# Optimization experiments

Hardware: AMD Instinct MI355X
Metric: run time of the kernel (lower is better)

The kernel has to match this reference:

```python
import jax, jax.numpy as jnp
import numpy as np

BLOCK_SPLIT = (4, 4, 4)
GRID = 256
N_BLOCK = 64
BX = GRID // 4  # 64, per-block grid resolution along each axis
N_PTS = 4_194_304


def setup_inputs() -> dict:
    key = jax.random.key(0)
    k1, k2 = jax.random.split(key)
    aabb = jnp.array([[-1.5, -1.5, -1.5], [1.5, 1.5, 1.5]], dtype=jnp.float32)
    # points roughly inside the aabb
    xyz_sampled = jax.random.uniform(k1, (N_PTS, 3), dtype=jnp.float32) * 3.0 - 1.5
    alpha_volume = jax.random.uniform(k2, (GRID, GRID, GRID), dtype=jnp.float32)
    # per-block domains (as kilonerf global_to_local expects): block AABBs
    idx = np.stack(np.meshgrid(np.arange(4), np.arange(4), np.arange(4), indexing='ij'), -1).reshape(-1, 3)
    voxel = np.array([3.0 / 4.0] * 3)
    dmin = (-1.5 + idx * voxel).astype(np.float32)
    dmax = (dmin + voxel).astype(np.float32)
    return {"xyz_sampled": xyz_sampled, "aabb": aabb, "alpha_volume": alpha_volume,
            "domain_min": jnp.asarray(dmin), "domain_max": jnp.asarray(dmax)}


def _sample_alpha(xyz, aabb, alpha_volume, dmin, dmax):
    bs = jnp.asarray(BLOCK_SPLIT, jnp.float32)
    voxel = (aabb[1] - aabb[0]) / bs                      # per-block world size
    idx3 = jnp.floor((xyz - aabb[0]) / voxel).astype(jnp.int32)
    idx3 = jnp.clip(idx3, 0, jnp.array(BLOCK_SPLIT, jnp.int32) - 1)  # edge clamp (matches loop)
    strides = jnp.array([BLOCK_SPLIT[2] * BLOCK_SPLIT[1], BLOCK_SPLIT[2], 1], jnp.int32)
    bid = (idx3 * strides).sum(-1)                        # [N] block id in [0, 64)

    order = jnp.argsort(bid)                              # jax sort is stable; matches bucket-by-block order
    bid_s = bid[order]
    pts = xyz[order]

    # global_to_local (kilonerf): map into per-block [-1,1]^3
    local = 2.0 * (pts - dmin[bid_s]) / (dmax[bid_s] - dmin[bid_s]) - 1.0  # [N,3] (gx,gy,gz)

    # torch .view(64,1,64,64,64) is a raw contiguous reinterpretation -> plain reshape
    vols = alpha_volume.reshape(N_BLOCK, BX, BX, BX)      # [B, D, H, W]
    D = H = W = BX
    # grid_sample convention: grid x -> W axis, y -> H axis, z -> D axis; align_corners=True
    fx = (local[:, 0] + 1.0) * 0.5 * (W - 1)
    fy = (local[:, 1] + 1.0) * 0.5 * (H - 1)
    fz = (local[:, 2] + 1.0) * 0.5 * (D - 1)
    x0 = jnp.floor(fx); y0 = jnp.floor(fy); z0 = jnp.floor(fz)
    wx = fx - x0; wy = fy - y0; wz = fz - z0
    x0i = x0.astype(jnp.int32); y0i = y0.astype(jnp.int32); z0i = z0.astype(jnp.int32)

    def fetch(zi, yi, xi):
        # zeros padding for out-of-range corners (grid_sample padding_mode='zeros')
        inb = (zi >= 0) & (zi < D) & (yi >= 0) & (yi < H) & (xi >= 0) & (xi < W)
        v = vols[bid_s, jnp.clip(zi, 0, D - 1), jnp.clip(yi, 0, H - 1), jnp.clip(xi, 0, W - 1)]
        return jnp.where(inb, v, 0.0)

    out = jnp.zeros_like(fx)
    for dz, wz_ in ((0, 1.0 - wz), (1, wz)):
        for dy, wy_ in ((0, 1.0 - wy), (1, wy)):
            for dx, wx_ in ((0, 1.0 - wx), (1, wx)):
                out = out + wz_ * wy_ * wx_ * fetch(z0i + dz, y0i + dy, x0i + dx)
    return out  # [N] alpha values in block-sorted order


def reference(xyz_sampled, aabb, alpha_volume, domain_min, domain_max):
    return _sample_alpha(xyz_sampled, aabb, alpha_volume, domain_min, domain_max)
```

## Files before the change

### kernel.cpp

```cpp
#include <hip/hip_runtime.h>

#define NB     64
#define NF     4096
#define TILE   16384
#define HBLK   1024
#define DBLK   1024
#define FBLK   512
#define GBLK   256
#define SBLK   256
#define FB_TILE 4096
#define STAGE_HALF 8192

#define GLOBAL_AS __attribute__((address_space(1)))
#define LDS_AS    __attribute__((address_space(3)))

__device__ __forceinline__ int compute_bid(float px, float py, float pz,
                                           float a0x, float a0y, float a0z,
                                           float vx, float vy, float vz) {
    int ix = (int)floorf((px - a0x) / vx);
    int iy = (int)floorf((py - a0y) / vy);
    int iz = (int)floorf((pz - a0z) / vz);
    ix = min(max(ix, 0), 3);
    iy = min(max(iy, 0), 3);
    iz = min(max(iz, 0), 3);
    return ix * 16 + iy * 4 + iz;
}

__device__ __forceinline__ void quant_point(float px, float py, float pz,
        float a0x, float a0y, float a0z, float vx, float vy, float vz,
        const float* s_dn, const float* s_sc,
        int& b, int& qx, int& qy, int& qz, int& key) {
    b = compute_bid(px, py, pz, a0x, a0y, a0z, vx, vy, vz);
    float fx = (px - s_dn[3 * b])     * s_sc[3 * b];
    float fy = (py - s_dn[3 * b + 1]) * s_sc[3 * b + 1];
    float fz = (pz - s_dn[3 * b + 2]) * s_sc[3 * b + 2];
    qx = min(max(__float2int_rn(fx * 256.0f), 0), 16128);
    qy = min(max(__float2int_rn(fy * 256.0f), 0), 16128);
    qz = min(max(__float2int_rn(fz * 256.0f), 0), 16128);
    key = (b << 6) | ((qz >> 12) << 4) | ((qy >> 12) << 2) | (qx >> 12);
}

__global__ void __launch_bounds__(HBLK) hist_kernel(
        const float* __restrict__ xyz, const float* __restrict__ aabb,
        const float* __restrict__ dmin, const float* __restrict__ dmax,
        int* __restrict__ hist64, int* __restrict__ tot4096, int N, int T) {
    __shared__ int   sh[NF];
    __shared__ float s_dn[192], s_sc[192];
    const int tid = threadIdx.x, g = blockIdx.x;
    for (int l = tid; l < NF; l += HBLK) sh[l] = 0;
    if (tid < 192) { s_dn[tid] = dmin[tid]; s_sc[tid] = 63.0f / (dmax[tid] - dmin[tid]); }
    const float a0x = aabb[0], a0y = aabb[1], a0z = aabb[2];
    const float vx = (aabb[3] - a0x) * 0.25f;
    const float vy = (aabb[4] - a0y) * 0.25f;
    const float vz = (aabb[5] - a0z) * 0.25f;
    __syncthreads();
    for (int c = 0; c < TILE / (HBLK * 4); ++c) {
        int p0 = g * TILE + c * (HBLK * 4) + tid * 4;
        int b, qx, qy, qz, k;
        if (p0 + 3 < N) {
            const float4* v4 = (const float4*)(xyz + (size_t)p0 * 3);
            float4 f0 = v4[0], f1 = v4[1], f2 = v4[2];
            quant_point(f0.x, f0.y, f0.z, a0x, a0y, a0z, vx, vy, vz, s_dn, s_sc, b, qx, qy, qz, k);
            atomicAdd(&sh[k], 1);
            quant_point(f0.w, f1.x, f1.y, a0x, a0y, a0z, vx, vy, vz, s_dn, s_sc, b, qx, qy, qz, k);
            atomicAdd(&sh[k], 1);
            quant_point(f1.z, f1.w, f2.x, a0x, a0y, a0z, vx, vy, vz, s_dn, s_sc, b, qx, qy, qz, k);
            atomicAdd(&sh[k], 1);
            quant_point(f2.y, f2.z, f2.w, a0x, a0y, a0z, vx, vy, vz, s_dn, s_sc, b, qx, qy, qz, k);
            atomicAdd(&sh[k], 1);
        } else {
            for (int t = 0; t < 4; ++t) {
                int i = p0 + t;
                if (i < N) {
                    quant_point(xyz[3 * i], xyz[3 * i + 1], xyz[3 * i + 2],
                                a0x, a0y, a0z, vx, vy, vz, s_dn, s_sc, b, qx, qy, qz, k);
                    atomicAdd(&sh[k], 1);
                }
            }
        }
    }
    __syncthreads();
    for (int l = tid; l < NF; l += HBLK) {
        int c = sh[l];
        if (c) atomicAdd(&tot4096[l], c);
    }
    if (tid < NB) {
        int s = 0;
        #pragma unroll
        for (int j = 0; j < 64; ++j) s += sh[tid * 64 + j];
        hist64[tid * T + g] = s;
    }
}

__global__ void scans_kernel(int* __restrict__ hist64, int* __restrict__ tot64,
                             const int* __restrict__ tot4096,
                             int* __restrict__ foff, int* __restrict__ fcnt, int G) {
    __shared__ int sh[SBLK];
    const int t = threadIdx.x;
    if (blockIdx.x < NB) {
        const int b = blockIdx.x;
        const int L = (G + SBLK - 1) / SBLK;
        const int lo = t * L;
        const int n = min(L, max(0, G - lo));
        const int base = b * G + lo;
        int s = 0;
        for (int k = 0; k < n; ++k) s += hist64[base + k];
        sh[t] = s;
        __syncthreads();
        for (int off = 1; off < SBLK; off <<= 1) {
            int v = (t >= off) ? sh[t - off] : 0;
            __syncthreads();
            sh[t] += v;
            __syncthreads();
        }
        int excl = (t == 0) ? 0 : sh[t - 1];
        for (int k = 0; k < n; ++k) {
            int v = hist64[base + k];
            hist64[base + k] = excl;
            excl += v;
        }
        if (t == SBLK - 1) tot64[b] = sh[SBLK - 1];
    } else {
        const int L = NF / SBLK;
        int loc[16];
        int s = 0;
        #pragma unroll
        for (int j = 0; j < L; ++j) { loc[j] = tot4096[t * L + j]; s += loc[j]; }
        sh[t] = s;
        __syncthreads();
        for (int o = 1; o < SBLK; o <<= 1) {
            int v = (t >= o) ? sh[t - o] : 0;
            __syncthreads();
            sh[t] += v;
            __syncthreads();
        }
        int run = (t == 0) ? 0 : sh[t - 1];
        #pragma unroll
        for (int j = 0; j < L; ++j) {
            foff[t * L + j] = run;
            fcnt[t * L + j] = run;
            run += loc[j];
        }
        if (t == SBLK - 1) foff[NF] = run;
    }
}

__global__ void __launch_bounds__(DBLK) scatterC_kernel(
        const float* __restrict__ xyz, const float* __restrict__ aabb,
        const float* __restrict__ dmin, const float* __restrict__ dmax,
        const int* __restrict__ hist64, const int* __restrict__ tot64,
        unsigned long long* __restrict__ payloadC, int N, int T) {
    __shared__ unsigned long long stage[STAGE_HALF];
    __shared__ int   s_wh[16][NB];
    __shared__ int   s_cnt0[NB];
    __shared__ int   s_off[NB];
    __shared__ int   s_start[NB];
    __shared__ int   s_gb[NB];
    __shared__ float s_dn[192], s_sc[192];
    const int tid = threadIdx.x, g = blockIdx.x;
    const int lane = tid & 63, wv = tid >> 6;
    if (tid < NB) s_off[tid] = tot64[tid];
    if (tid < 192) { s_dn[tid] = dmin[tid]; s_sc[tid] = 63.0f / (dmax[tid] - dmin[tid]); }
    ((int*)s_wh)[tid] = 0;
    const float a0x = aabb[0], a0y = aabb[1], a0z = aabb[2];
    const float vx = (aabb[3] - a0x) * 0.25f;
    const float vy = (aabb[4] - a0y) * 0.25f;
    const float vz = (aabb[5] - a0z) * 0.25f;
    __syncthreads();
    for (int o = 1; o < NB; o <<= 1) {
        int v = (tid < NB && tid >= o) ? s_off[tid - o] : 0;
        __syncthreads();
        if (tid < NB) s_off[tid] += v;
        __syncthreads();
    }
    if (tid < NB) s_cnt0[tid] = hist64[tid * T + g] + (tid ? s_off[tid - 1] : 0);

    const unsigned long long lt = (1ull << lane) - 1ull;
    const int base_i = g * TILE + wv * 1024;
    unsigned long long cache[16];
    #pragma unroll
    for (int r = 0; r < 16; ++r) {
        int i = base_i + r * 64 + lane;
        bool valid = (i < N);
        int b = 0, qx = 0, qy = 0, qz = 0, key;
        if (valid) {
            quant_point(xyz[3 * i], xyz[3 * i + 1], xyz[3 * i + 2],
                        a0x, a0y, a0z, vx, vy, vz, s_dn, s_sc, b, qx, qy, qz, key);
        }
        unsigned long long m = __ballot(valid);
        #pragma unroll
        for (int q = 0; q < 6; ++q) {
            unsigned long long bal = __ballot((b >> q) & 1);
            m &= ((b >> q) & 1) ? bal : ~bal;
        }
        int rank = __popcll(m & lt);
        int run = valid ? s_wh[wv][b] : 0;
        if (valid && rank == 0) s_wh[wv][b] = run + __popcll(m);
        int localpos = run + rank;
        cache[r] = (unsigned long long)(unsigned)qx
                 | ((unsigned long long)(unsigned)qy << 14)
                 | ((unsigned long long)(unsigned)qz << 28)
                 | ((unsigned long long)(unsigned)b  << 42)
                 | ((unsigned long long)(unsigned)localpos << 48);
    }
    __syncthreads();
    for (int o = 1; o < 16; o <<= 1) {
        int v = (wv >= o) ? s_wh[wv - o][lane] : 0;
        __syncthreads();
        s_wh[wv][lane] += v;
        __syncthreads();
    }
    if (wv == 0) {
        int v = s_wh[15][lane];
        int incl = v;
        #pragma unroll
        for (int o = 1; o < 64; o <<= 1) {
            int u = __shfl_up(incl, o);
            if (lane >= o) incl += u;
        }
        int excl = incl - v;
        s_start[lane] = excl;
        s_gb[lane] = s_cnt0[lane] - excl;
    }
    __syncthreads();
    const int n = min(TILE, N - g * TILE);
    #pragma unroll
    for (int r = 0; r < 16; ++r) {
        int i = base_i + r * 64 + lane;
        if (i < N) {
            unsigned long long cc = cache[r];
            int b = (int)((cc >> 42) & 63);
            int localpos = (int)((cc >> 48) & 1023);
            int lidx = s_start[b] + (wv ? s_wh[wv - 1][b] : 0) + localpos;
            unsigned long long p48 = cc & ((1ull << 48) - 1);
            if (lidx < STAGE_HALF) stage[lidx] = p48;
            cache[r] = p48 | ((unsigned long long)(unsigned)lidx << 48);
        }
    }
    __syncthreads();
    {
        int nA = min(n, STAGE_HALF);
        for (int j = tid; j < nA; j += DBLK) {
            unsigned long long p = stage[j];
            int b = (int)((p >> 42) & 63);
            payloadC[s_gb[b] + j] = p;
        }
    }
    __syncthreads();
    #pragma unroll
    for (int r = 0; r < 16; ++r) {
        int i = base_i + r * 64 + lane;
        if (i < N) {
            unsigned long long cc = cache[r];
            int lidx = (int)(cc >> 48);
            if (lidx >= STAGE_HALF)
                stage[lidx - STAGE_HALF] = cc & ((1ull << 48) - 1);
        }
    }
    __syncthreads();
    for (int j = STAGE_HALF + tid; j < n; j += DBLK) {
        unsigned long long p = stage[j - STAGE_HALF];
        int b = (int)((p >> 42) & 63);
        payloadC[s_gb[b] + j] = p;
    }
}

__global__ void __launch_bounds__(FBLK) scatterF_kernel(
        const unsigned long long* __restrict__ payloadC,
        int* __restrict__ fcnt,
        unsigned long long* __restrict__ payloadF, int N) {
    __shared__ int s_fb[NF];
    const int tid = threadIdx.x, t2 = blockIdx.x;
    for (int l = tid; l < NF; l += FBLK) s_fb[l] = 0;
    __syncthreads();
    const int lo = t2 * TILE;
    const int n = min(TILE, N - lo);
    for (int j = tid; j < n; j += FBLK) {
        unsigned long long p = payloadC[lo + j];
        int qx = (int)(p & 16383), qy = (int)((p >> 14) & 16383);
        int qz = (int)((p >> 28) & 16383), b = (int)((p >> 42) & 63);
        int key = (b << 6) | ((qz >> 12) << 4) | ((qy >> 12) << 2) | (qx >> 12);
        atomicAdd(&s_fb[key], 1);
    }
    __syncthreads();
    for (int l = tid; l < NF; l += FBLK) {
        int c = s_fb[l];
        s_fb[l] = c ? atomicAdd(&fcnt[l], c) : 0;
    }
    __syncthreads();
    for (int j = tid; j < n; j += FBLK) {
        unsigned long long p = payloadC[lo + j];
        int qx = (int)(p & 16383), qy = (int)((p >> 14) & 16383);
        int qz = (int)((p >> 28) & 16383), b = (int)((p >> 42) & 63);
        int key = (b << 6) | ((qz >> 12) << 4) | ((qy >> 12) << 2) | (qx >> 12);
        int fpos = atomicAdd(&s_fb[key], 1);
        payloadF[fpos] = (p & ((1ull << 42) - 1))
                       | ((unsigned long long)(unsigned)(lo + j) << 42);
    }
}

__global__ void __launch_bounds__(GBLK) gather_kernel(
        const float* __restrict__ vol,
        const unsigned long long* __restrict__ payloadF,
        const int* __restrict__ foff, const float* __restrict__ zf,
        float* __restrict__ out) {
    __shared__ float sv[77 * 64];
    const int tid = threadIdx.x;
    const int lane = tid & 63, wv = tid >> 6;
    const int nb = gridDim.x, d = blockIdx.x;
    const int k = (nb % 8 == 0) ? (d % 8) * (nb / 8) + (d / 8) : d;
    const int b = k >> 6;
    const int bz = ((k >> 4) & 3) * 16, by = ((k >> 2) & 3) * 16, bx = (k & 3) * 16;
    const float* vb = vol + ((size_t)b << 18);
    for (int m = wv; m < 77; m += GBLK / 64) {
        int l = m * 64 + lane;
        int z = l / 289, r = l - z * 289, y = r / 17, x = r - y * 17;
        int gz = bz + z, gy = by + y, gx = bx + x;
        bool ok = (l < 17 * 17 * 17) && (gz < 64) && (gy < 64) && (gx < 64);
        const float* src = ok ? (vb + ((gz << 12) + (gy << 6) + gx)) : zf;
        __builtin_amdgcn_global_load_lds((const GLOBAL_AS void*)src,
                                         (LDS_AS void*)(sv + m * 64), 4, 0, 0);
    }
    __syncthreads();
    const int lo = foff[k];
    const int n = foff[k + 1] - lo;
    for (int j = tid; j < n; j += GBLK) {
        unsigned long long p = payloadF[lo + j];
        int qx = (int)(p & 16383), qy = (int)((p >> 14) & 16383);
        int qz = (int)((p >> 28) & 16383);
        int pos = (int)(p >> 42);
        float wx = (qx & 255) * (1.0f / 256.0f);
        float wy = (qy & 255) * (1.0f / 256.0f);
        float wz = (qz & 255) * (1.0f / 256.0f);
        int lx = (qx >> 8) - bx, ly = (qy >> 8) - by, lz = (qz >> 8) - bz;
        int base = lz * 289 + ly * 17 + lx;
        float v000 = sv[base],       v001 = sv[base + 1];
        float v010 = sv[base + 17],  v011 = sv[base + 18];
        float v100 = sv[base + 289], v101 = sv[base + 290];
        float v110 = sv[base + 306], v111 = sv[base + 307];
        float c00 = v000 + wx * (v001 - v000);
        float c01 = v010 + wx * (v011 - v010);
        float c10 = v100 + wx * (v101 - v100);
        float c11 = v110 + wx * (v111 - v110);
        float c0 = c00 + wy * (c01 - c00);
        float c1 = c10 + wy * (c11 - c10);
        out[pos] = c0 + wz * (c1 - c0);
    }
}

__global__ void fb_hist_kernel(const float* __restrict__ xyz,
                               const float* __restrict__ aabb,
                               int* __restrict__ hist, int N, int G) {
    __shared__ int s_h[NB];
    const int tid = threadIdx.x, g = blockIdx.x;
    if (tid < NB) s_h[tid] = 0;
    __syncthreads();
    const float a0x = aabb[0], a0y = aabb[1], a0z = aabb[2];
    const float vx = (aabb[3] - a0x) * 0.25f;
    const float vy = (aabb[4] - a0y) * 0.25f;
    const float vz = (aabb[5] - a0z) * 0.25f;
    for (int c = 0; c < FB_TILE / 256; ++c) {
        int i = g * FB_TILE + c * 256 + tid;
        if (i < N)
            atomicAdd(&s_h[compute_bid(xyz[3 * i], xyz[3 * i + 1], xyz[3 * i + 2],
                                       a0x, a0y, a0z, vx, vy, vz)], 1);
    }
    __syncthreads();
    if (tid < NB) hist[tid * G + g] = s_h[tid];
}

__global__ void fb_scan_kernel(int* __restrict__ hist, int* __restrict__ tot, int G) {
    __shared__ int sh[SBLK];
    const int b = blockIdx.x, t = threadIdx.x;
    const int L = (G + SBLK - 1) / SBLK;
    const int lo = t * L;
    const int n = min(L, max(0, G - lo));
    const int base = b * G + lo;
    int s = 0;
    for (int k = 0; k < n; ++k) s += hist[base + k];
    sh[t] = s;
    __syncthreads();
    for (int off = 1; off < SBLK; off <<= 1) {
        int v = (t >= off) ? sh[t - off] : 0;
        __syncthreads();
        sh[t] += v;
        __syncthreads();
    }
    int excl = (t == 0) ? 0 : sh[t - 1];
    for (int k = 0; k < n; ++k) {
        int v = hist[base + k];
        hist[base + k] = excl;
        excl += v;
    }
    if (t == SBLK - 1) tot[b] = sh[SBLK - 1];
}

__global__ void fb_scatter_kernel(const float* __restrict__ xyz,
                                  const float* __restrict__ aabb,
                                  const float* __restrict__ dmin,
                                  const float* __restrict__ dmax,
                                  const float* __restrict__ vol,
                                  const int* __restrict__ hist,
                                  const int* __restrict__ tot64,
                                  float* __restrict__ out, int N, int G) {
    __shared__ int   s_cnt[NB], s_off[NB];
    __shared__ int   s_whist[4][NB];
    __shared__ float s_dn[192], s_sc[192];
    const int tid = threadIdx.x, g = blockIdx.x;
    if (tid < NB) s_off[tid] = tot64[tid];
    if (tid < 192) { s_dn[tid] = dmin[tid]; s_sc[tid] = 63.0f / (dmax[tid] - dmin[tid]); }
    __syncthreads();
    for (int o = 1; o < NB; o <<= 1) {
        int v = (tid < NB && tid >= o) ? s_off[tid - o] : 0;
        __syncthreads();
        if (tid < NB) s_off[tid] += v;
        __syncthreads();
    }
    if (tid < NB) s_cnt[tid] = hist[tid * G + g] + (tid ? s_off[tid - 1] : 0);
    const float a0x = aabb[0], a0y = aabb[1], a0z = aabb[2];
    const float vx = (aabb[3] - a0x) * 0.25f;
    const float vy = (aabb[4] - a0y) * 0.25f;
    const float vz = (aabb[5] - a0z) * 0.25f;
    __syncthreads();
    const int lane = tid & 63, wv = tid >> 6;
    const unsigned long long lt = (1ull << lane) - 1ull;
    for (int c = 0; c < FB_TILE / 256; ++c) {
        int i = g * FB_TILE + c * 256 + tid;
        bool valid = (i < N);
        int b = 0;
        float alpha = 0.0f;
        if (valid) {
            float px = xyz[3 * i], py = xyz[3 * i + 1], pz = xyz[3 * i + 2];
            b = compute_bid(px, py, pz, a0x, a0y, a0z, vx, vy, vz);
            float fx = (px - s_dn[3 * b])     * s_sc[3 * b];
            float fy = (py - s_dn[3 * b + 1]) * s_sc[3 * b + 1];
            float fz = (pz - s_dn[3 * b + 2]) * s_sc[3 * b + 2];
            float x0f = floorf(fx), y0f = floorf(fy), z0f = floorf(fz);
            float wx = fx - x0f, wy = fy - y0f, wz = fz - z0f;
            int x0 = (int)x0f, y0 = (int)y0f, z0 = (int)z0f;
            const float* vb = vol + ((size_t)b << 18);
            auto F = [&](int zi, int yi, int xi) -> float {
                if ((unsigned)zi >= 64u || (unsigned)yi >= 64u || (unsigned)xi >= 64u)
                    return 0.0f;
                return vb[(zi << 12) + (yi << 6) + xi];
            };
            float s = 0.0f;
            s += (1.0f - wz) * (1.0f - wy) * (1.0f - wx) * F(z0,     y0,     x0);
            s += (1.0f - wz) * (1.0f - wy) * wx          * F(z0,     y0,     x0 + 1);
            s += (1.0f - wz) * wy          * (1.0f - wx) * F(z0,     y0 + 1, x0);
            s += (1.0f - wz) * wy          * wx          * F(z0,     y0 + 1, x0 + 1);
            s += wz          * (1.0f - wy) * (1.0f - wx) * F(z0 + 1, y0,     x0);
            s += wz          * (1.0f - wy) * wx          * F(z0 + 1, y0,     x0 + 1);
            s += wz          * wy          * (1.0f - wx) * F(z0 + 1, y0 + 1, x0);
            s += wz          * wy          * wx          * F(z0 + 1, y0 + 1, x0 + 1);
            alpha = s;
        }
        ((int*)s_whist)[tid] = 0;
        __syncthreads();
        unsigned long long m = __ballot(valid);
        #pragma unroll
        for (int q = 0; q < 6; ++q) {
            unsigned long long bal = __ballot((b >> q) & 1);
            m &= ((b >> q) & 1) ? bal : ~bal;
        }
        int rank = __popcll(m & lt);
        if (valid && rank == 0) s_whist[wv][b] = __popcll(m);
        __syncthreads();
        if (valid) {
            int pos = s_cnt[b] + rank;
            for (int w2 = 0; w2 < wv; ++w2) pos += s_whist[w2][b];
            out[pos] = alpha;
        }
        __syncthreads();
        if (tid < NB)
            s_cnt[tid] += s_whist[0][tid] + s_whist[1][tid] +
                          s_whist[2][tid] + s_whist[3][tid];
        __syncthreads();
    }
}

extern "C" void kernel_launch(void* const* d_in, const int* in_sizes, int n_in,
                              void* d_out, int out_size, void* d_ws, size_t ws_size,
                              hipStream_t stream) {
    const float* xyz  = (const float*)d_in[0];
    const float* aabb = (const float*)d_in[1];
    const float* vol  = (const float*)d_in[2];
    const float* dmin = (const float*)d_in[3];
    const float* dmax = (const float*)d_in[4];
    float* out = (float*)d_out;
    const int N = in_sizes[0] / 3;
    const int T = (N + TILE - 1) / TILE;

    auto align = [](size_t x) { return (x + 255) & ~(size_t)255; };
    char* ws = (char*)d_ws;
    size_t o = 0;
    unsigned long long* payloadC = (unsigned long long*)(ws + o); o += align((size_t)N * 8);
    unsigned long long* payloadF = (unsigned long long*)(ws + o); o += align((size_t)N * 8);
    int* hist64  = (int*)(ws + o); o += align((size_t)NB * T * 4);
    int* tot64   = (int*)(ws + o); o += 256;
    size_t zbase = o;
    int* tot4096 = (int*)(ws + o); o += align((size_t)NF * 4);
    int* foff    = (int*)(ws + o); o += align((size_t)(NF + 1) * 4);
    int* fcnt    = (int*)(ws + o); o += align((size_t)NF * 4);
    float* zf    = (float*)(ws + o); o += 256;
    size_t zlen = o - zbase;
    const bool fine = (N <= (1 << 22)) && (ws_size >= o);

    if (fine) {
        hipMemsetAsync(ws + zbase, 0, zlen, stream);
        hist_kernel<<<T, HBLK, 0, stream>>>(xyz, aabb, dmin, dmax,
                                            hist64, tot4096, N, T);
        scans_kernel<<<NB + 1, SBLK, 0, stream>>>(hist64, tot64, tot4096,
                                                  foff, fcnt, T);
        scatterC_kernel<<<T, DBLK, 0, stream>>>(xyz, aabb, dmin, dmax,
                                                hist64, tot64, payloadC, N, T);
        scatterF_kernel<<<T, FBLK, 0, stream>>>(payloadC, fcnt, payloadF, N);
        gather_kernel<<<NF, GBLK, 0, stream>>>(vol, payloadF, foff, zf, out);
    } else {
        const int Gf = (N + FB_TILE - 1) / FB_TILE;
        int* h = (int*)ws;
        int* t = (int*)(ws + align((size_t)NB * Gf * 4));
        fb_hist_kernel<<<Gf, 256, 0, stream>>>(xyz, aabb, h, N, Gf);
        fb_scan_kernel<<<NB, SBLK, 0, stream>>>(h, t, Gf);
        fb_scatter_kernel<<<Gf, 256, 0, stream>>>(xyz, aabb, dmin, dmax, vol,
                                                  h, t, out, N, Gf);
    }
}
```

Measured before the change: 260.0 us.

## Double-buffer LDS tiles in gather kernel, four x-cells per workgroup

The gather kernel now has each workgroup walk four consecutive x-cells of a block, with the LDS tile held in two buffers. The next cell's tile is loaded asynchronously with global_load_lds while the current cell's points are interpolated. The aim is to hide the tile-load latency behind compute and to cut the number of workgroups launched by a factor of four. In exchange, fewer workgroups (1024) may reduce parallelism across CUs, LDS use doubles, and an extra barrier is added per cell.

After: 265.4 us. +2.1%, slower.

```diff
diff --git a/kernel.cpp b/kernel.cpp
--- a/kernel.cpp
+++ b/kernel.cpp
@@ -10,6 +10,7 @@
 #define SBLK   256
 #define FB_TILE 4096
 #define STAGE_HALF 8192
+#define GCELLS 4
 
 #define GLOBAL_AS __attribute__((address_space(1)))
 #define LDS_AS    __attribute__((address_space(3)))
@@ -304,47 +305,61 @@
         const unsigned long long* __restrict__ payloadF,
         const int* __restrict__ foff, const float* __restrict__ zf,
         float* __restrict__ out) {
-    __shared__ float sv[77 * 64];
+    __shared__ float sv[2][77 * 64];
     const int tid = threadIdx.x;
     const int lane = tid & 63, wv = tid >> 6;
-    const int nb = gridDim.x, d = blockIdx.x;
-    const int k = (nb % 8 == 0) ? (d % 8) * (nb / 8) + (d / 8) : d;
-    const int b = k >> 6;
-    const int bz = ((k >> 4) & 3) * 16, by = ((k >> 2) & 3) * 16, bx = (k & 3) * 16;
+    const int nbn = gridDim.x, d = blockIdx.x;
+    const int g = (nbn % 8 == 0) ? (d % 8) * (nbn / 8) + (d / 8) : d;
+    const int b = g >> 4;
+    const int bz = ((g >> 2) & 3) * 16, by = (g & 3) * 16;
     const float* vb = vol + ((size_t)b << 18);
-    for (int m = wv; m < 77; m += GBLK / 64) {
-        int l = m * 64 + lane;
-        int z = l / 289, r = l - z * 289, y = r / 17, x = r - y * 17;
-        int gz = bz + z, gy = by + y, gx = bx + x;
-        bool ok = (l < 17 * 17 * 17) && (gz < 64) && (gy < 64) && (gx < 64);
-        const float* src = ok ? (vb + ((gz << 12) + (gy << 6) + gx)) : zf;
-        __builtin_amdgcn_global_load_lds((const GLOBAL_AS void*)src,
-                                         (LDS_AS void*)(sv + m * 64), 4, 0, 0);
-    }
-    __syncthreads();
-    const int lo = foff[k];
-    const int n = foff[k + 1] - lo;
-    for (int j = tid; j < n; j += GBLK) {
-        unsigned long long p = payloadF[lo + j];
-        int qx = (int)(p & 16383), qy = (int)((p >> 14) & 16383);
-        int qz = (int)((p >> 28) & 16383);
-        int pos = (int)(p >> 42);
-        float wx = (qx & 255) * (1.0f / 256.0f);
-        float wy = (qy & 255) * (1.0f / 256.0f);
-        float wz = (qz & 255) * (1.0f / 256.0f);
-        int lx = (qx >> 8) - bx, ly = (qy >> 8) - by, lz = (qz >> 8) - bz;
-        int base = lz * 289 + ly * 17 + lx;
-        float v000 = sv[base],       v001 = sv[base + 1];
-        float v010 = sv[base + 17],  v011 = sv[base + 18];
-        float v100 = sv[base + 289], v101 = sv[base + 290];
-        float v110 = sv[base + 306], v111 = sv[base + 307];
-        float c00 = v000 + wx * (v001 - v000);
-        float c01 = v010 + wx * (v011 - v010);
-        float c10 = v100 + wx * (v101 - v100);
-        float c11 = v110 + wx * (v111 - v110);
-        float c0 = c00 + wy * (c01 - c00);
-        float c1 = c10 + wy * (c11 - c10);
-        out[pos] = c0 + wz * (c1 - c0);
+
+    auto STAGE = [&](int c) {
+        const int bx = c * 16;
+        float* dst = sv[c & 1];
+        for (int m = wv; m < 77; m += GBLK / 64) {
+            int l = m * 64 + lane;
+            int z = l / 289, r = l - z * 289, y = r / 17, x = r - y * 17;
+            int gz = bz + z, gy = by + y, gx = bx + x;
+            bool ok = (l < 17 * 17 * 17) && (gz < 64) && (gy < 64) && (gx < 64);
+            const float* src = ok ? (vb + ((gz << 12) + (gy << 6) + gx)) : zf;
+            __builtin_amdgcn_global_load_lds((const GLOBAL_AS void*)src,
+                                             (LDS_AS void*)(dst + m * 64), 4, 0, 0);
+        }
+    };
+
+    STAGE(0);
+    __syncthreads();
+    for (int c = 0; c < GCELLS; ++c) {
+        if (c + 1 < GCELLS) STAGE(c + 1);
+        const int k = g * GCELLS + c;
+        const int bx = c * 16;
+        const float* s = sv[c & 1];
+        const int lo = foff[k];
+        const int n = foff[k + 1] - lo;
+        for (int j = tid; j < n; j += GBLK) {
+            unsigned long long p = payloadF[lo + j];
+            int qx = (int)(p & 16383), qy = (int)((p >> 14) & 16383);
+            int qz = (int)((p >> 28) & 16383);
+            int pos = (int)(p >> 42);
+            float wx = (qx & 255) * (1.0f / 256.0f);
+            float wy = (qy & 255) * (1.0f / 256.0f);
+            float wz = (qz & 255) * (1.0f / 256.0f);
+            int lx = (qx >> 8) - bx, ly = (qy >> 8) - by, lz = (qz >> 8) - bz;
+            int base = lz * 289 + ly * 17 + lx;
+            float v000 = s[base],       v001 = s[base + 1];
+            float v010 = s[base + 17],  v011 = s[base + 18];
+            float v100 = s[base + 289], v101 = s[base + 290];
+            float v110 = s[base + 306], v111 = s[base + 307];
+            float c00 = v000 + wx * (v001 - v000);
+            float c01 = v010 + wx * (v011 - v010);
+            float c10 = v100 + wx * (v101 - v100);
+            float c11 = v110 + wx * (v111 - v110);
+            float c0 = c00 + wy * (c01 - c00);
+            float c1 = c10 + wy * (c11 - c10);
+            out[pos] = c0 + wz * (c1 - c0);
+        }
+        __syncthreads();
     }
 }
 
@@ -515,7 +530,7 @@
         scatterC_kernel<<<T, DBLK, 0, stream>>>(xyz, aabb, dmin, dmax,
                                                 hist64, tot64, payloadC, N, T);
         scatterF_kernel<<<T, FBLK, 0, stream>>>(payloadC, fcnt, payloadF, N);
-        gather_kernel<<<NF, GBLK, 0, stream>>>(vol, payloadF, foff, zf, out);
+        gather_kernel<<<NF / GCELLS, GBLK, 0, stream>>>(vol, payloadF, foff, zf, out);
     } else {
         const int Gf = (N + FB_TILE - 1) / FB_TILE;
         int* h = (int*)ws;
```
